# Performance work log

Hardware: AMD Instinct MI355X
Metric: run time of the kernel (lower is better)

Reference implementation:

```python
import jax, jax.numpy as jnp
import numpy as np

B, K, C, O = 8, 100000, 16, 16
HG, WG = 512, 512
ALPHA_PRIOR = 1.0
KERN = np.array([[0.075, 0.125, 0.075], [0.125, 0.3, 0.125], [0.075, 0.125, 0.075]], dtype=np.float32)


def setup_inputs() -> dict:
    key = jax.random.key(0)
    k1, k2, k3, k4, k5 = jax.random.split(key, 5)
    node_feat = jax.random.normal(k1, (B, K, C), dtype=jnp.float32)
    node_xy = jax.random.uniform(k2, (B, K, 2), dtype=jnp.float32, minval=0.0, maxval=WG - 1.0)
    node_types = jax.random.randint(k3, (B, K), 0, 2)
    # kaiming_normal_ fan_out: std = sqrt(2 / fan_out), fan_out = O*1*1
    std = (2.0 / O) ** 0.5
    w_obj = jax.random.normal(k4, (O, C), dtype=jnp.float32) * std
    w_prior = jax.random.normal(k5, (O, C), dtype=jnp.float32) * std
    hw = np.array([HG, WG], dtype=np.int64)
    return {"node_feat": node_feat, "node_xy": node_xy, "hw": hw,
            "node_types": node_types, "w_obj": w_obj, "w_prior": w_prior}


def rasterize(node_feat, node_xy, weight, H, W):
    # node_feat [B,K,C], node_xy [B,K,2], weight [B,K] 0/1 mask (masked scatter == scatter of zeros)
    xs = jnp.clip(jnp.round(node_xy[..., 0]), 0, W - 1).astype(jnp.int32)
    ys = jnp.clip(jnp.round(node_xy[..., 1]), 0, H - 1).astype(jnp.int32)
    idx = ys * W + xs  # [B,K] flat grid index
    src = node_feat * weight[..., None]  # zero out non-selected nodes

    def scat(idx_b, src_b):
        return jnp.zeros((H * W, src_b.shape[-1]), src_b.dtype).at[idx_b].add(src_b)

    grid = jax.vmap(scat)(idx, src)  # [B,HW,C]
    return grid.reshape(grid.shape[0], H, W, -1).transpose(0, 3, 1, 2)  # [B,C,H,W]


def splat3x3(x, kern):
    # depthwise 3x3 conv, groups = C
    c = x.shape[1]
    w = jnp.broadcast_to(kern[None, None], (c, 1, 3, 3))
    return jax.lax.conv_general_dilated(
        x, w, window_strides=(1, 1), padding='SAME',
        dimension_numbers=('NCHW', 'OIHW', 'NCHW'), feature_group_count=c)


def reference(node_feat, node_xy, hw, node_types, w_obj, w_prior):
    H, W = int(hw[0]), int(hw[1])
    kern = jnp.asarray(KERN)
    mask_obj = (node_types == 0).astype(node_feat.dtype)
    mask_prior = (node_types == 1).astype(node_feat.dtype)
    map_obj = splat3x3(rasterize(node_feat, node_xy, mask_obj, H, W), kern)
    map_prior = splat3x3(rasterize(node_feat, node_xy, mask_prior, H, W), kern)
    # rasterize + splat run under torch.no_grad() in the original
    map_obj = jax.lax.stop_gradient(map_obj)
    map_prior = jax.lax.stop_gradient(map_prior)
    out = jnp.einsum('oc,bchw->bohw', w_obj, map_obj) \
        + ALPHA_PRIOR * jnp.einsum('oc,bchw->bohw', w_prior, map_prior)
    return out
```

## Files before the change

### kernel.cpp

```cpp
#include <hip/hip_runtime.h>

#define B_ 8
#define K_ 100000
#define NODES (B_ * K_)
#define C_ 16
#define O_ 16
#define H_ 512
#define W_ 512
#define TSX 32
#define TSY 16
#define NTX (W_ / TSX)
#define NTY (H_ / TSY)
#define NBKT (B_ * NTX * NTY)
#define CAP 512
#define EX (TSX + 2)
#define EY (TSY + 2)
#define PLANE (EX * EY)
#define FB 256
#define FCHUNK (K_ / (FB / B_))
#define IDS_OFF 16384

__device__ __forceinline__ float bf_lo(unsigned int u) {
    union { unsigned int i; float f; } v; v.i = u << 16; return v.f;
}
__device__ __forceinline__ float bf_hi(unsigned int u) {
    union { unsigned int i; float f; } v; v.i = u & 0xffff0000u; return v.f;
}
__device__ __forceinline__ unsigned short f2bf(float f) {
    union { float f; unsigned int u; } v; v.f = f;
    unsigned int u = v.u;
    u += 0x7fffu + ((u >> 16) & 1u);
    return (unsigned short)(u >> 16);
}

__device__ __forceinline__ void probe_fp32(const unsigned int* xy, int tid,
                                           int* bad )
{
    if (tid == 0) *bad = 0;
    if (tid < 256) {
        float lo = bf_lo(xy[tid]);
        if (!(lo >= 0.0f && lo <= 512.0f)) *bad = 1;
    }
}

__device__ __forceinline__ void decode_xy(const void* xy, int fp32, int n,
                                          int& xs, int& ys)
{
    float x, y;
    if (fp32) { float2 p = ((const float2*)xy)[n]; x = p.x; y = p.y; }
    else { unsigned int u = ((const unsigned int*)xy)[n]; x = bf_lo(u); y = bf_hi(u); }
    xs = min(max((int)rintf(x), 0), W_ - 1);
    ys = min(max((int)rintf(y), 0), H_ - 1);
}

__global__ __launch_bounds__(256) void fill_bins(
    const void* __restrict__ xy, const int* __restrict__ types,
    int* __restrict__ cursor, int* __restrict__ ids)
{
    __shared__ int hist[NTX * NTY];
    __shared__ unsigned int rec[FCHUNK];
    __shared__ int bad;

    const int tid = threadIdx.x;
    probe_fp32((const unsigned int*)xy, tid, &bad);
    for (int j = tid; j < NTX * NTY; j += 256) hist[j] = 0;
    __syncthreads();
    const int fp32 = bad;

    const int bb = blockIdx.x >> 5;
    const int local0 = (blockIdx.x & 31) * FCHUNK;
    const int s = bb * K_ + local0;

    for (int ii = tid; ii < FCHUNK; ii += 256) {
        int n = s + ii;
        int xs, ys; decode_xy(xy, fp32, n, xs, ys);
        int t = (types[n] != 0);
        rec[ii] = (unsigned)(xs | (ys << 9) | (t << 18));
        int xlo = max((xs - 1) >> 5, 0), xhi = min((xs + 1) >> 5, NTX - 1);
        int ylo = max((ys - 1) >> 4, 0), yhi = min((ys + 1) >> 4, NTY - 1);
        for (int tyy = ylo; tyy <= yhi; ++tyy)
            for (int txx = xlo; txx <= xhi; ++txx)
                atomicAdd(&hist[tyy * NTX + txx], 1);
    }
    __syncthreads();

    for (int j = tid; j < NTX * NTY; j += 256) {
        int c = hist[j];
        hist[j] = c ? atomicAdd(&cursor[bb * NTX * NTY + j], c) : 0;
    }
    __syncthreads();

    for (int ii = tid; ii < FCHUNK; ii += 256) {
        unsigned r = rec[ii];
        int xs = r & 511, ys = (r >> 9) & 511, t = (r >> 18) & 1;
        int local = local0 + ii;
        int xlo = max((xs - 1) >> 5, 0), xhi = min((xs + 1) >> 5, NTX - 1);
        int ylo = max((ys - 1) >> 4, 0), yhi = min((ys + 1) >> 4, NTY - 1);
        for (int tyy = ylo; tyy <= yhi; ++tyy)
            for (int txx = xlo; txx <= xhi; ++txx) {
                int bk = tyy * NTX + txx;
                int slot = atomicAdd(&hist[bk], 1);
                if (slot < CAP) {
                    int lx = xs - (txx << 5) + 1;
                    int ly = ys - (tyy << 4) + 1;
                    ids[(bb * NTX * NTY + bk) * CAP + slot] =
                        local | (t << 17) | (lx << 18) | (ly << 24);
                }
            }
    }
}

__global__ __launch_bounds__(512) void tile_fused(
    const void* __restrict__ feat, const void* __restrict__ xy,
    const void* __restrict__ w_obj, const void* __restrict__ w_prior,
    const int* __restrict__ cursor, const int* __restrict__ ids,
    void* __restrict__ out)
{
    __shared__ float accs[O_ * PLANE];
    __shared__ float wl[2 * O_ * C_];
    __shared__ int bad;

    const int tid = threadIdx.x;
    const int tx = blockIdx.x, ty = blockIdx.y, b = blockIdx.z;
    const int bucket = (b * NTY + ty) * NTX + tx;
    int cnt = cursor[bucket];
    if (cnt > CAP) cnt = CAP;

    probe_fp32((const unsigned int*)xy, tid, &bad);
    for (int i = tid; i < O_ * PLANE; i += 512) accs[i] = 0.f;
    __syncthreads();
    const int fp32 = bad;

    if (fp32) {
        for (int i = tid; i < 2 * O_ * C_; i += 512)
            wl[i] = (i < O_ * C_) ? ((const float*)w_obj)[i]
                                  : ((const float*)w_prior)[i - O_ * C_];
    } else {
        for (int i = tid; i < 2 * O_ * C_; i += 512) {
            unsigned short raw = (i < O_ * C_)
                ? ((const unsigned short*)w_obj)[i]
                : ((const unsigned short*)w_prior)[i - O_ * C_];
            union { unsigned int u; float f; } v; v.u = ((unsigned int)raw) << 16;
            wl[i] = v.f;
        }
    }
    __syncthreads();

    for (int i = tid; i < cnt; i += 512) {
        unsigned p = (unsigned)ids[bucket * CAP + i];
        int local = p & 0x1FFFF;
        int t  = (p >> 17) & 1;
        int lx = (p >> 18) & 63;
        int ly = (p >> 24) & 31;
        size_t n = (size_t)b * K_ + local;

        float f[16];
        if (fp32) {
            const float4* ff = (const float4*)feat + n * 4;
            float4 a = ff[0], bb2 = ff[1], c = ff[2], d = ff[3];
            f[0]=a.x; f[1]=a.y; f[2]=a.z; f[3]=a.w;
            f[4]=bb2.x; f[5]=bb2.y; f[6]=bb2.z; f[7]=bb2.w;
            f[8]=c.x; f[9]=c.y; f[10]=c.z; f[11]=c.w;
            f[12]=d.x; f[13]=d.y; f[14]=d.z; f[15]=d.w;
        } else {
            const uint4* ff = (const uint4*)feat + n * 2;
            uint4 A = ff[0], Bv = ff[1];
            f[0]=bf_lo(A.x);  f[1]=bf_hi(A.x);  f[2]=bf_lo(A.y);  f[3]=bf_hi(A.y);
            f[4]=bf_lo(A.z);  f[5]=bf_hi(A.z);  f[6]=bf_lo(A.w);  f[7]=bf_hi(A.w);
            f[8]=bf_lo(Bv.x); f[9]=bf_hi(Bv.x); f[10]=bf_lo(Bv.y); f[11]=bf_hi(Bv.y);
            f[12]=bf_lo(Bv.z); f[13]=bf_hi(Bv.z); f[14]=bf_lo(Bv.w); f[15]=bf_hi(Bv.w);
        }

        const float* wrow = &wl[t * O_ * C_];
        float* cell = &accs[ly * EX + lx];
        #pragma unroll
        for (int o = 0; o < O_; ++o) {
            float acc = 0.f;
            #pragma unroll
            for (int c = 0; c < C_; ++c) acc = fmaf(wrow[o * C_ + c], f[c], acc);
            atomicAdd(cell + o * PLANE, acc);
        }
    }
    __syncthreads();

    const int x = tid & 31;
    const int o = tid >> 5;
    const float* pl = &accs[o * PLANE + x];
    float hA2 = 0.f, hA1 = 0.f, hB1 = 0.f;
    const int x0 = tx * TSX, y0 = ty * TSY;
    const size_t obase = (((size_t)(b * O_ + o)) * H_) * W_;

    #pragma unroll
    for (int iy = 0; iy < EY; ++iy) {
        float l = pl[iy * EX], c = pl[iy * EX + 1], r = pl[iy * EX + 2];
        float sfx = l + r;
        float hA = fmaf(0.075f, sfx, 0.125f * c);
        float hB = fmaf(0.125f, sfx, 0.3f * c);
        if (iy >= 2) {
            float v = hA2 + hB1 + hA;
            size_t oi = obase + (size_t)(y0 + iy - 2) * W_ + (x0 + x);
            if (fp32) __builtin_nontemporal_store(v, (float*)out + oi);
            else      __builtin_nontemporal_store(f2bf(v), (unsigned short*)out + oi);
        }
        hA2 = hA1; hA1 = hA; hB1 = hB;
    }
}

extern "C" void kernel_launch(void* const* d_in, const int* in_sizes, int n_in,
                              void* d_out, int out_size, void* d_ws, size_t ws_size,
                              hipStream_t stream)
{
    const void* feat = d_in[0];
    const void* xy = d_in[1];
    const int* types = (const int*)d_in[3];
    const void* w_obj = d_in[4];
    const void* w_prior = d_in[5];

    int* cursor = (int*)d_ws;
    int* ids = (int*)((char*)d_ws + IDS_OFF);

    hipMemsetAsync(cursor, 0, NBKT * sizeof(int), stream);
    fill_bins<<<FB, 256, 0, stream>>>(xy, types, cursor, ids);
    tile_fused<<<dim3(NTX, NTY, B_), 512, 0, stream>>>(
        feat, xy, w_obj, w_prior, cursor, ids, d_out);
}
```

Measured before the change: 287.0 us.

## Precompute per-node projections in binning pass and simplify tile accumulation

The 16x16 channel projection moves from the tile kernel, where each node was projected up to four times because of halo duplication, into the binning kernel, which projects each node once and writes the result to a workspace buffer. The binning grid grows to 1000 blocks for more parallelism. The shared-memory fp32 probe becomes a wavefront ballot. The tile kernel now handles one node per thread and starts its gather loads before the shared-memory zeroing barrier. This adds a write and re-read of a node-by-16 float buffer. The new path runs only when the workspace is large enough, and it assumes at most 512 nodes per bucket, which matches CAP.

Result: no change. 285.3 us (-0.6%).

```diff
diff --git a/kernel.cpp b/kernel.cpp
--- a/kernel.cpp
+++ b/kernel.cpp
@@ -16,9 +16,12 @@
 #define EX (TSX + 2)
 #define EY (TSY + 2)
 #define PLANE (EX * EY)
-#define FB 256
-#define FCHUNK (K_ / (FB / B_))
+#define FB 1000
+#define FPB (FB / B_)
+#define FCHUNK (K_ / FPB)
 #define IDS_OFF 16384
+#define P_OFF (IDS_OFF + NBKT * CAP * 4)
+#define WS_NEED ((size_t)P_OFF + (size_t)NODES * O_ * 4)
 
 __device__ __forceinline__ float bf_lo(unsigned int u) {
     union { unsigned int i; float f; } v; v.i = u << 16; return v.f;
@@ -33,14 +36,15 @@
     return (unsigned short)(u >> 16);
 }
 
-__device__ __forceinline__ void probe_fp32(const unsigned int* xy, int tid,
-                                           int* bad )
-{
-    if (tid == 0) *bad = 0;
-    if (tid < 256) {
-        float lo = bf_lo(xy[tid]);
-        if (!(lo >= 0.0f && lo <= 512.0f)) *bad = 1;
-    }
+__device__ __forceinline__ int probe_fp32_ballot(const unsigned int* xy) {
+    const int lane = threadIdx.x & 63;
+    int bad = 0;
+    #pragma unroll
+    for (int k = 0; k < 4; ++k) {
+        float lo = bf_lo(xy[lane + (k << 6)]);
+        bad |= !(lo >= 0.0f && lo <= 512.0f);
+    }
+    return __ballot(bad) != 0ull;
 }
 
 __device__ __forceinline__ void decode_xy(const void* xy, int fp32, int n,
@@ -53,29 +57,79 @@
     ys = min(max((int)rintf(y), 0), H_ - 1);
 }
 
+template<bool PRE>
 __global__ __launch_bounds__(256) void fill_bins(
-    const void* __restrict__ xy, const int* __restrict__ types,
-    int* __restrict__ cursor, int* __restrict__ ids)
+    const void* __restrict__ feat, const void* __restrict__ xy,
+    const int* __restrict__ types,
+    const void* __restrict__ w_obj, const void* __restrict__ w_prior,
+    int* __restrict__ cursor, int* __restrict__ ids, float* __restrict__ p)
 {
     __shared__ int hist[NTX * NTY];
     __shared__ unsigned int rec[FCHUNK];
-    __shared__ int bad;
+    __shared__ float wl[PRE ? 2 * O_ * C_ : 2];
 
     const int tid = threadIdx.x;
-    probe_fp32((const unsigned int*)xy, tid, &bad);
+    const int fp32 = probe_fp32_ballot((const unsigned int*)xy);
     for (int j = tid; j < NTX * NTY; j += 256) hist[j] = 0;
-    __syncthreads();
-    const int fp32 = bad;
-
-    const int bb = blockIdx.x >> 5;
-    const int local0 = (blockIdx.x & 31) * FCHUNK;
+    if constexpr (PRE) {
+        for (int i = tid; i < 2 * O_ * C_; i += 256) {
+            if (fp32) {
+                wl[i] = (i < O_ * C_) ? ((const float*)w_obj)[i]
+                                      : ((const float*)w_prior)[i - O_ * C_];
+            } else {
+                unsigned short raw = (i < O_ * C_)
+                    ? ((const unsigned short*)w_obj)[i]
+                    : ((const unsigned short*)w_prior)[i - O_ * C_];
+                union { unsigned int u; float f; } v; v.u = ((unsigned int)raw) << 16;
+                wl[i] = v.f;
+            }
+        }
+    }
+    __syncthreads();
+
+    const int bb = blockIdx.x / FPB;
+    const int local0 = (blockIdx.x % FPB) * FCHUNK;
     const int s = bb * K_ + local0;
 
     for (int ii = tid; ii < FCHUNK; ii += 256) {
-        int n = s + ii;
+        const int n = s + ii;
         int xs, ys; decode_xy(xy, fp32, n, xs, ys);
-        int t = (types[n] != 0);
+        const int t = (types[n] != 0);
         rec[ii] = (unsigned)(xs | (ys << 9) | (t << 18));
+
+        if constexpr (PRE) {
+            float f[16];
+            if (fp32) {
+                const float4* ff = (const float4*)feat + (size_t)n * 4;
+                float4 a = ff[0], b2 = ff[1], c = ff[2], d = ff[3];
+                f[0]=a.x; f[1]=a.y; f[2]=a.z; f[3]=a.w;
+                f[4]=b2.x; f[5]=b2.y; f[6]=b2.z; f[7]=b2.w;
+                f[8]=c.x; f[9]=c.y; f[10]=c.z; f[11]=c.w;
+                f[12]=d.x; f[13]=d.y; f[14]=d.z; f[15]=d.w;
+            } else {
+                const uint4* ff = (const uint4*)feat + (size_t)n * 2;
+                uint4 A = ff[0], Bv = ff[1];
+                f[0]=bf_lo(A.x);  f[1]=bf_hi(A.x);  f[2]=bf_lo(A.y);  f[3]=bf_hi(A.y);
+                f[4]=bf_lo(A.z);  f[5]=bf_hi(A.z);  f[6]=bf_lo(A.w);  f[7]=bf_hi(A.w);
+                f[8]=bf_lo(Bv.x); f[9]=bf_hi(Bv.x); f[10]=bf_lo(Bv.y); f[11]=bf_hi(Bv.y);
+                f[12]=bf_lo(Bv.z); f[13]=bf_hi(Bv.z); f[14]=bf_lo(Bv.w); f[15]=bf_hi(Bv.w);
+            }
+            const float* wrow = &wl[t * O_ * C_];
+            float pv[16];
+            #pragma unroll
+            for (int o = 0; o < O_; ++o) {
+                float acc = 0.f;
+                #pragma unroll
+                for (int c = 0; c < C_; ++c) acc = fmaf(wrow[o * C_ + c], f[c], acc);
+                pv[o] = acc;
+            }
+            float4* pout = (float4*)(p + (size_t)n * O_);
+            pout[0] = make_float4(pv[0],  pv[1],  pv[2],  pv[3]);
+            pout[1] = make_float4(pv[4],  pv[5],  pv[6],  pv[7]);
+            pout[2] = make_float4(pv[8],  pv[9],  pv[10], pv[11]);
+            pout[3] = make_float4(pv[12], pv[13], pv[14], pv[15]);
+        }
+
         int xlo = max((xs - 1) >> 5, 0), xhi = min((xs + 1) >> 5, NTX - 1);
         int ylo = max((ys - 1) >> 4, 0), yhi = min((ys + 1) >> 4, NTY - 1);
         for (int tyy = ylo; tyy <= yhi; ++tyy)
@@ -110,75 +164,92 @@
     }
 }
 
+template<bool PRE>
 __global__ __launch_bounds__(512) void tile_fused(
-    const void* __restrict__ feat, const void* __restrict__ xy,
+    const void* __restrict__ src ,
+    const void* __restrict__ xy,
     const void* __restrict__ w_obj, const void* __restrict__ w_prior,
     const int* __restrict__ cursor, const int* __restrict__ ids,
     void* __restrict__ out)
 {
     __shared__ float accs[O_ * PLANE];
-    __shared__ float wl[2 * O_ * C_];
-    __shared__ int bad;
+    __shared__ float wl[PRE ? 2 : 2 * O_ * C_];
 
     const int tid = threadIdx.x;
     const int tx = blockIdx.x, ty = blockIdx.y, b = blockIdx.z;
     const int bucket = (b * NTY + ty) * NTX + tx;
     int cnt = cursor[bucket];
     if (cnt > CAP) cnt = CAP;
-
-    probe_fp32((const unsigned int*)xy, tid, &bad);
-    for (int i = tid; i < O_ * PLANE; i += 512) accs[i] = 0.f;
-    __syncthreads();
-    const int fp32 = bad;
-
-    if (fp32) {
-        for (int i = tid; i < 2 * O_ * C_; i += 512)
-            wl[i] = (i < O_ * C_) ? ((const float*)w_obj)[i]
-                                  : ((const float*)w_prior)[i - O_ * C_];
-    } else {
-        for (int i = tid; i < 2 * O_ * C_; i += 512) {
-            unsigned short raw = (i < O_ * C_)
-                ? ((const unsigned short*)w_obj)[i]
-                : ((const unsigned short*)w_prior)[i - O_ * C_];
-            union { unsigned int u; float f; } v; v.u = ((unsigned int)raw) << 16;
-            wl[i] = v.f;
-        }
-    }
-    __syncthreads();
-
-    for (int i = tid; i < cnt; i += 512) {
-        unsigned p = (unsigned)ids[bucket * CAP + i];
-        int local = p & 0x1FFFF;
-        int t  = (p >> 17) & 1;
-        int lx = (p >> 18) & 63;
-        int ly = (p >> 24) & 31;
-        size_t n = (size_t)b * K_ + local;
-
-        float f[16];
-        if (fp32) {
-            const float4* ff = (const float4*)feat + n * 4;
-            float4 a = ff[0], bb2 = ff[1], c = ff[2], d = ff[3];
+    const int fp32 = probe_fp32_ballot((const unsigned int*)xy);
+
+    float f[16];
+    int t = 0, lx = 0, ly = 0;
+    const bool active = (tid < cnt);
+    if (active) {
+        const unsigned pck = (unsigned)ids[bucket * CAP + tid];
+        const int local = pck & 0x1FFFF;
+        t  = (pck >> 17) & 1;
+        lx = (pck >> 18) & 63;
+        ly = (pck >> 24) & 31;
+        const size_t n = (size_t)b * K_ + local;
+        if constexpr (PRE) {
+            const float4* pp = (const float4*)src + n * 4;
+            float4 a = pp[0], b2 = pp[1], c = pp[2], d = pp[3];
             f[0]=a.x; f[1]=a.y; f[2]=a.z; f[3]=a.w;
-            f[4]=bb2.x; f[5]=bb2.y; f[6]=bb2.z; f[7]=bb2.w;
+            f[4]=b2.x; f[5]=b2.y; f[6]=b2.z; f[7]=b2.w;
             f[8]=c.x; f[9]=c.y; f[10]=c.z; f[11]=c.w;
             f[12]=d.x; f[13]=d.y; f[14]=d.z; f[15]=d.w;
         } else {
-            const uint4* ff = (const uint4*)feat + n * 2;
-            uint4 A = ff[0], Bv = ff[1];
-            f[0]=bf_lo(A.x);  f[1]=bf_hi(A.x);  f[2]=bf_lo(A.y);  f[3]=bf_hi(A.y);
-            f[4]=bf_lo(A.z);  f[5]=bf_hi(A.z);  f[6]=bf_lo(A.w);  f[7]=bf_hi(A.w);
-            f[8]=bf_lo(Bv.x); f[9]=bf_hi(Bv.x); f[10]=bf_lo(Bv.y); f[11]=bf_hi(Bv.y);
-            f[12]=bf_lo(Bv.z); f[13]=bf_hi(Bv.z); f[14]=bf_lo(Bv.w); f[15]=bf_hi(Bv.w);
-        }
-
-        const float* wrow = &wl[t * O_ * C_];
+            if (fp32) {
+                const float4* ff = (const float4*)src + n * 4;
+                float4 a = ff[0], b2 = ff[1], c = ff[2], d = ff[3];
+                f[0]=a.x; f[1]=a.y; f[2]=a.z; f[3]=a.w;
+                f[4]=b2.x; f[5]=b2.y; f[6]=b2.z; f[7]=b2.w;
+                f[8]=c.x; f[9]=c.y; f[10]=c.z; f[11]=c.w;
+                f[12]=d.x; f[13]=d.y; f[14]=d.z; f[15]=d.w;
+            } else {
+                const uint4* ff = (const uint4*)src + n * 2;
+                uint4 A = ff[0], Bv = ff[1];
+                f[0]=bf_lo(A.x);  f[1]=bf_hi(A.x);  f[2]=bf_lo(A.y);  f[3]=bf_hi(A.y);
+                f[4]=bf_lo(A.z);  f[5]=bf_hi(A.z);  f[6]=bf_lo(A.w);  f[7]=bf_hi(A.w);
+                f[8]=bf_lo(Bv.x); f[9]=bf_hi(Bv.x); f[10]=bf_lo(Bv.y); f[11]=bf_hi(Bv.y);
+                f[12]=bf_lo(Bv.z); f[13]=bf_hi(Bv.z); f[14]=bf_lo(Bv.w); f[15]=bf_hi(Bv.w);
+            }
+        }
+    }
+
+    for (int i = tid; i < O_ * PLANE; i += 512) accs[i] = 0.f;
+    if constexpr (!PRE) {
+        if (fp32) {
+            for (int i = tid; i < 2 * O_ * C_; i += 512)
+                wl[i] = (i < O_ * C_) ? ((const float*)w_obj)[i]
+                                      : ((const float*)w_prior)[i - O_ * C_];
+        } else {
+            for (int i = tid; i < 2 * O_ * C_; i += 512) {
+                unsigned short raw = (i < O_ * C_)
+                    ? ((const unsigned short*)w_obj)[i]
+                    : ((const unsigned short*)w_prior)[i - O_ * C_];
+                union { unsigned int u; float f; } v; v.u = ((unsigned int)raw) << 16;
+                wl[i] = v.f;
+            }
+        }
+    }
+    __syncthreads();
+
+    if (active) {
         float* cell = &accs[ly * EX + lx];
-        #pragma unroll
-        for (int o = 0; o < O_; ++o) {
-            float acc = 0.f;
+        if constexpr (PRE) {
             #pragma unroll
-            for (int c = 0; c < C_; ++c) acc = fmaf(wrow[o * C_ + c], f[c], acc);
-            atomicAdd(cell + o * PLANE, acc);
+            for (int o = 0; o < O_; ++o) atomicAdd(cell + o * PLANE, f[o]);
+        } else {
+            const float* wrow = &wl[t * O_ * C_];
+            #pragma unroll
+            for (int o = 0; o < O_; ++o) {
+                float acc = 0.f;
+                #pragma unroll
+                for (int c = 0; c < C_; ++c) acc = fmaf(wrow[o * C_ + c], f[c], acc);
+                atomicAdd(cell + o * PLANE, acc);
+            }
         }
     }
     __syncthreads();
@@ -218,9 +289,18 @@
 
     int* cursor = (int*)d_ws;
     int* ids = (int*)((char*)d_ws + IDS_OFF);
+    float* p = (float*)((char*)d_ws + P_OFF);
 
     hipMemsetAsync(cursor, 0, NBKT * sizeof(int), stream);
-    fill_bins<<<FB, 256, 0, stream>>>(xy, types, cursor, ids);
-    tile_fused<<<dim3(NTX, NTY, B_), 512, 0, stream>>>(
-        feat, xy, w_obj, w_prior, cursor, ids, d_out);
-}
+    if (ws_size >= WS_NEED) {
+        fill_bins<true><<<FB, 256, 0, stream>>>(feat, xy, types, w_obj, w_prior,
+                                                cursor, ids, p);
+        tile_fused<true><<<dim3(NTX, NTY, B_), 512, 0, stream>>>(
+            p, xy, w_obj, w_prior, cursor, ids, d_out);
+    } else {
+        fill_bins<false><<<FB, 256, 0, stream>>>(feat, xy, types, w_obj, w_prior,
+                                                 cursor, ids, p);
+        tile_fused<false><<<dim3(NTX, NTY, B_), 512, 0, stream>>>(
+            feat, xy, w_obj, w_prior, cursor, ids, d_out);
+    }
+}
```
